# Kernel tuning notes

Hardware: AMD Instinct MI355X
Metric: run time of the kernel (lower is better)

The kernel has to match this reference:

```python
import jax, jax.numpy as jnp
import numpy as np

B, C, HEADS, DH = 2, 1280, 20, 64
INNER = HEADS * DH
HW = 64
S = HW * HW
L = 77
ENC = 4096
GROUPS = 32
EPS = 1e-5
CREG = 1.0     # creg_ in __init__
NOATTN = 1.0   # global noattn
NORES = 1.0    # global noresidual


def setup_inputs() -> dict:
    key = jax.random.key(0)
    ks = jax.random.split(key, 10)
    std = 0.02
    return {
        "x": jax.random.normal(ks[0], (B, C, HW, HW), jnp.float32),
        "text": jax.random.normal(ks[1], (B, L, ENC), jnp.float32),
        "gn_gamma": jnp.ones((C,), jnp.float32),
        "gn_beta": jnp.zeros((C,), jnp.float32),
        "ln_gamma": jnp.ones((ENC,), jnp.float32),
        "ln_beta": jnp.zeros((ENC,), jnp.float32),
        "Wq": jax.random.normal(ks[2], (C, INNER), jnp.float32) * std,
        "bq": jnp.zeros((INNER,), jnp.float32),
        "Wk": jax.random.normal(ks[3], (ENC, INNER), jnp.float32) * std,
        "bk": jnp.zeros((INNER,), jnp.float32),
        "Wv": jax.random.normal(ks[4], (ENC, INNER), jnp.float32) * std,
        "bv": jnp.zeros((INNER,), jnp.float32),
        "Wo": jax.random.normal(ks[5], (INNER, C), jnp.float32) * std,
        "bo": jnp.zeros((C,), jnp.float32),
        "size_reg": jax.random.uniform(ks[6], (1, S, L), jnp.float32),
        "treg": jax.random.uniform(ks[7], (1,), jnp.float32),
        "mask": jax.random.randint(ks[8], (1, S, L), 0, 2, jnp.int32),
    }


def _group_norm(h, gamma, beta):
    # h: [B, C, S]; GroupNorm over (C//GROUPS, S) per group
    hg = h.reshape(B, GROUPS, -1)
    mu = hg.mean(-1, keepdims=True)
    var = hg.var(-1, keepdims=True)
    hn = ((hg - mu) * jax.lax.rsqrt(var + EPS)).reshape(B, C, S)
    return hn * gamma[None, :, None] + beta[None, :, None]


def _layer_norm(t, gamma, beta):
    mu = t.mean(-1, keepdims=True)
    var = t.var(-1, keepdims=True)
    return (t - mu) * jax.lax.rsqrt(var + EPS) * gamma + beta


def reference(x, text, gn_gamma, gn_beta, ln_gamma, ln_beta, Wq, bq, Wk, bk,
              Wv, bv, Wo, bo, size_reg, treg, mask):
    residual = x                              # [B, C, HW, HW]
    h = x.reshape(B, C, S)                    # spatial tokens
    h = _group_norm(h, gn_gamma, gn_beta).transpose(0, 2, 1)   # [B, S, C]
    enc = _layer_norm(text, ln_gamma, ln_beta)                  # [B, L, ENC]

    # head_to_batch_dim (out_dim=3): [B, T, inner] -> [B*heads, T, dh]
    q = (h @ Wq + bq).reshape(B, S, HEADS, DH).transpose(0, 2, 1, 3).reshape(B * HEADS, S, DH)
    k = (enc @ Wk + bk).reshape(B, L, HEADS, DH).transpose(0, 2, 1, 3).reshape(B * HEADS, L, DH)
    v = (enc @ Wv + bv).reshape(B, L, HEADS, DH).transpose(0, 2, 1, 3).reshape(B * HEADS, L, DH)

    scale = DH ** -0.5
    sim = jnp.einsum('bsd,bld->bsl', q, k) * scale            # [B*H, S, L]

    # region regularization applied only to the conditional (second) half
    half = (B * HEADS) // 2
    sim_u, sim_c = sim[:half], sim[half:]
    mn = sim_c.min(-1, keepdims=True)
    mx = sim_c.max(-1, keepdims=True)
    m = mask > 0                                               # [1, S, L] broadcasts over heads
    w = size_reg * CREG * treg[0]
    sim_c = sim_c + jnp.where(m, w, 0.0) * (mx - sim_c) - jnp.where(m, 0.0, w) * (sim_c - mn)
    sim = jnp.concatenate([sim_u, sim_c], axis=0)

    probs = jax.nn.softmax(sim, axis=-1)
    out = jnp.einsum('bsl,bld->bsd', probs, v)                 # [B*H, S, DH]
    # batch_to_head_dim: [B*H, S, DH] -> [B, S, inner]
    out = out.reshape(B, HEADS, S, DH).transpose(0, 2, 1, 3).reshape(B, S, INNER)
    out = out @ Wo + bo                                        # to_out[0]; dropout p=0
    out = out.transpose(0, 2, 1).reshape(residual.shape)       # [B, C, HW, HW]
    return out * NOATTN + residual * NORES
```

## Files before the change

kernel.cpp:

```cpp
#include <hip/hip_runtime.h>

typedef __bf16 bf16_t;
typedef __bf16 bf16x8 __attribute__((ext_vector_type(8)));
typedef float  f32x4  __attribute__((ext_vector_type(4)));
typedef unsigned int u32x4 __attribute__((ext_vector_type(4)));


__global__ __launch_bounds__(256) void k_transpose_cvt2(
    const float* __restrict__ in0, const float* __restrict__ in1,
    bf16_t* __restrict__ out0, bf16_t* __restrict__ out1, int R, int C)
{
  const float* in  = blockIdx.z ? in1 : in0;
  bf16_t*      out = blockIdx.z ? out1 : out0;
  __shared__ float tile[64][33];
  const int c0 = blockIdx.x * 32, r0 = blockIdx.y * 64;
  const int t = threadIdx.x;
#pragma unroll
  for (int it = 0; it < 8; ++it) {
    int r = it * 8 + (t >> 5), c = t & 31;
    tile[r][c] = in[(size_t)(r0 + r) * C + c0 + c];
  }
  __syncthreads();
  {
    const int oc  = t >> 3;
    const int seg = t & 7;
    bf16x8 o;
#pragma unroll
    for (int e = 0; e < 8; ++e) o[e] = (bf16_t)tile[seg * 8 + e][oc];
    *(bf16x8*)(out + (size_t)(c0 + oc) * R + r0 + seg * 8) = o;
  }
}

__global__ __launch_bounds__(256) void k_gn_partial(
    const float* __restrict__ x, float* __restrict__ partial)
{
  const int bg    = blockIdx.x >> 5;
  const int chunk = blockIdx.x & 31;
  const float* p  = x + (size_t)bg * 163840 + (size_t)chunk * 5120;
  float s1 = 0.f, s2 = 0.f;
#pragma unroll
  for (int it = 0; it < 5; ++it) {
    float4 v = *(const float4*)(p + (size_t)(it * 256 + threadIdx.x) * 4);
    s1 += v.x + v.y + v.z + v.w;
    s2 += v.x * v.x + v.y * v.y + v.z * v.z + v.w * v.w;
  }
#pragma unroll
  for (int off = 32; off > 0; off >>= 1) {
    s1 += __shfl_down(s1, off);
    s2 += __shfl_down(s2, off);
  }
  __shared__ float r1[4], r2[4];
  if ((threadIdx.x & 63) == 0) { r1[threadIdx.x >> 6] = s1; r2[threadIdx.x >> 6] = s2; }
  __syncthreads();
  if (threadIdx.x == 0) {
    partial[blockIdx.x * 2]     = r1[0] + r1[1] + r1[2] + r1[3];
    partial[blockIdx.x * 2 + 1] = r2[0] + r2[1] + r2[2] + r2[3];
  }
}

__global__ __launch_bounds__(64) void k_gn_finalize(
    const float* __restrict__ partial, float* __restrict__ stats)
{
  const int bg = threadIdx.x;
  float t1 = 0.f, t2 = 0.f;
#pragma unroll
  for (int c = 0; c < 32; ++c) {
    t1 += partial[(bg * 32 + c) * 2];
    t2 += partial[(bg * 32 + c) * 2 + 1];
  }
  const float invN = 1.0f / 163840.0f;
  float mu  = t1 * invN;
  float var = t2 * invN - mu * mu;
  stats[bg * 2]     = mu;
  stats[bg * 2 + 1] = rsqrtf(var + 1e-5f);
}

__global__ __launch_bounds__(256) void k_gn_apply(
    const float* __restrict__ x, const float* __restrict__ stats,
    const float* __restrict__ gamma, const float* __restrict__ beta,
    bf16_t* __restrict__ h)
{
  __shared__ float tile[64][65];
  const int s0 = blockIdx.x * 64;
  const int c0 = blockIdx.y * 64;
  const int b  = blockIdx.z;
  const int t  = threadIdx.x;
#pragma unroll
  for (int it = 0; it < 16; ++it) {
    int cl = it * 4 + (t >> 6);
    int sl = t & 63;
    tile[cl][sl] = x[((size_t)(b * 1280 + c0 + cl) << 12) + s0 + sl];
  }
  __syncthreads();
#pragma unroll
  for (int it = 0; it < 2; ++it) {
    int i  = it * 256 + t;
    int sl = i >> 3;
    int cg = i & 7;
    bf16x8 o;
#pragma unroll
    for (int e = 0; e < 8; ++e) {
      int c  = c0 + cg * 8 + e;
      int g  = c / 40;
      float mu = stats[(b * 32 + g) * 2];
      float rs = stats[(b * 32 + g) * 2 + 1];
      o[e] = (bf16_t)((tile[cg * 8 + e][sl] - mu) * rs * gamma[c] + beta[c]);
    }
    *(bf16x8*)(h + (size_t)(b * 4096 + s0 + sl) * 1280 + c0 + cg * 8) = o;
  }
}

__global__ __launch_bounds__(256) void k_ln(
    const float* __restrict__ text, const float* __restrict__ g,
    const float* __restrict__ bta, bf16_t* __restrict__ enc)
{
  const int row = blockIdx.x;
  const float* p = text + (size_t)row * 4096;
  float s1 = 0.f, s2 = 0.f;
  for (int i = threadIdx.x; i < 1024; i += 256) {
    float4 v = *(const float4*)(p + (size_t)i * 4);
    s1 += v.x + v.y + v.z + v.w;
    s2 += v.x * v.x + v.y * v.y + v.z * v.z + v.w * v.w;
  }
#pragma unroll
  for (int off = 32; off > 0; off >>= 1) {
    s1 += __shfl_down(s1, off);
    s2 += __shfl_down(s2, off);
  }
  __shared__ float r1[4], r2[4], sh[2];
  if ((threadIdx.x & 63) == 0) { r1[threadIdx.x >> 6] = s1; r2[threadIdx.x >> 6] = s2; }
  __syncthreads();
  if (threadIdx.x == 0) {
    float t1 = r1[0] + r1[1] + r1[2] + r1[3];
    float t2 = r2[0] + r2[1] + r2[2] + r2[3];
    const float invN = 1.0f / 4096.0f;
    float mu  = t1 * invN;
    float var = t2 * invN - mu * mu;
    sh[0] = mu;
    sh[1] = rsqrtf(var + 1e-5f);
  }
  __syncthreads();
  const float mu = sh[0], rs = sh[1];
  for (int i = threadIdx.x; i < 1024; i += 256) {
    float4 v  = *(const float4*)(p + (size_t)i * 4);
    float4 gg = *(const float4*)(g + (size_t)i * 4);
    float4 bb = *(const float4*)(bta + (size_t)i * 4);
    bf16_t* o = enc + (size_t)row * 4096 + (size_t)i * 4;
    o[0] = (bf16_t)((v.x - mu) * rs * gg.x + bb.x);
    o[1] = (bf16_t)((v.y - mu) * rs * gg.y + bb.y);
    o[2] = (bf16_t)((v.z - mu) * rs * gg.z + bb.z);
    o[3] = (bf16_t)((v.w - mu) * rs * gg.w + bb.w);
  }
}

template <int EPI>
__global__ __launch_bounds__(256) void k_gemm(
    const bf16_t* __restrict__ A, const bf16_t* __restrict__ BT,
    const float* __restrict__ bias, bf16_t* __restrict__ outb,
    float* __restrict__ outf, const float* __restrict__ xres,
    float* __restrict__ dout, int M, int lda, int klen)
{
  __shared__ alignas(16) bf16_t smem[4][128 * 64];
  const int tid  = threadIdx.x;
  const int lane = tid & 63;
  const int wv   = tid >> 6;
  const int wm   = wv >> 1, wn = wv & 1;
  const int m0   = blockIdx.x * 128;
  const int n0   = blockIdx.y * 128;
  const int kbeg = blockIdx.z * klen;

  f32x4 acc[4][4];
  const f32x4 fz = {0.f, 0.f, 0.f, 0.f};
#pragma unroll
  for (int i = 0; i < 4; ++i)
#pragma unroll
    for (int j = 0; j < 4; ++j) acc[i][j] = fz;

  auto stage = [&](int buf, int kt) {
#pragma unroll
    for (int it = 0; it < 4; ++it) {
      int slot = it * 256 + tid;
      int row  = slot >> 3, ch = slot & 7;
      int grow = m0 + row; if (grow > M - 1) grow = M - 1;
      const bf16_t* ga = A  + (size_t)grow * lda + kt + ((ch ^ (row & 7)) << 3);
      const bf16_t* gb = BT + (size_t)(n0 + row) * lda + kt + ((ch ^ (row & 7)) << 3);
      __builtin_amdgcn_global_load_lds(
          (const __attribute__((address_space(1))) void*)ga,
          (__attribute__((address_space(3))) void*)((char*)&smem[buf * 2][0] + slot * 16),
          16, 0, 0);
      __builtin_amdgcn_global_load_lds(
          (const __attribute__((address_space(1))) void*)gb,
          (__attribute__((address_space(3))) void*)((char*)&smem[buf * 2 + 1][0] + slot * 16),
          16, 0, 0);
    }
  };

  const int nt = klen >> 6;
  stage(0, kbeg);
  if (nt > 1) stage(1, kbeg + 64);

  for (int t = 0; t < nt; ++t) {
    if (t + 1 < nt) { asm volatile("s_waitcnt vmcnt(8)" ::: "memory"); }
    else            { asm volatile("s_waitcnt vmcnt(0)" ::: "memory"); }
    __builtin_amdgcn_s_barrier();
    const char* pA = (const char*)&smem[(t & 1) * 2][0];
    const char* pB = (const char*)&smem[(t & 1) * 2 + 1][0];
#pragma unroll
    for (int ks = 0; ks < 2; ++ks) {
      const int kb = ks * 64 + ((lane >> 4) << 4);
      bf16x8 af[4], bfg[4];
#pragma unroll
      for (int i = 0; i < 4; ++i) {
        int r = wm * 64 + i * 16 + (lane & 15);
        af[i]  = *(const bf16x8*)(pA + r * 128 + (kb ^ ((r & 7) << 4)));
        int c = wn * 64 + i * 16 + (lane & 15);
        bfg[i] = *(const bf16x8*)(pB + c * 128 + (kb ^ ((c & 7) << 4)));
      }
#pragma unroll
      for (int i = 0; i < 4; ++i)
#pragma unroll
        for (int j = 0; j < 4; ++j)
          acc[i][j] = __builtin_amdgcn_mfma_f32_16x16x32_bf16(af[i], bfg[j], acc[i][j], 0, 0, 0);
    }
    asm volatile("s_waitcnt lgkmcnt(0)" ::: "memory");
    __builtin_amdgcn_s_barrier();
    if (t + 2 < nt) stage(t & 1, kbeg + (t + 2) * 64);
  }

  if (EPI == 0) {
    bf16_t* cst = &smem[0][0];
#pragma unroll
    for (int j = 0; j < 4; ++j) {
      const int n  = n0 + wn * 64 + j * 16 + (lane & 15);
      const float bs = bias[n];
      const int cl = wn * 64 + j * 16 + (lane & 15);
#pragma unroll
      for (int i = 0; i < 4; ++i) {
        const int rl = wm * 64 + i * 16 + ((lane >> 4) << 2);
#pragma unroll
        for (int r = 0; r < 4; ++r)
          cst[(rl + r) * 144 + cl] = (bf16_t)(acc[i][j][r] + bs);
      }
    }
    __syncthreads();
#pragma unroll
    for (int it = 0; it < 8; ++it) {
      int slot = it * 256 + tid;
      int row = slot >> 4, ch = slot & 15;
      u32x4 d = *(const u32x4*)(cst + row * 144 + ch * 8);
      *(u32x4*)(outb + (size_t)(m0 + row) * 1280 + n0 + ch * 8) = d;
    }
  } else {
#pragma unroll
    for (int i = 0; i < 4; ++i) {
      const int mrow = m0 + wm * 64 + i * 16 + ((lane >> 4) << 2);
#pragma unroll
      for (int j = 0; j < 4; ++j) {
        const int n = n0 + wn * 64 + j * 16 + (lane & 15);
        if (EPI == 2) {
          const int b = mrow >> 12, s = mrow & 4095;
          const size_t off = ((size_t)(b * 1280 + n) << 12) + s;
          const float bs = bias[n];
          const float4 xr = *(const float4*)(xres + off);
          float4 o;
          o.x = acc[i][j][0] + bs + xr.x;
          o.y = acc[i][j][1] + bs + xr.y;
          o.z = acc[i][j][2] + bs + xr.z;
          o.w = acc[i][j][3] + bs + xr.w;
          *(float4*)(dout + off) = o;
        } else {
#pragma unroll
          for (int r = 0; r < 4; ++r)
            if (mrow + r < M)
              outf[(size_t)blockIdx.z * (154 * 1280) + (size_t)(mrow + r) * 1280 + n] = acc[i][j][r];
        }
      }
    }
  }
}

__global__ __launch_bounds__(256) void k_kv_reduce(
    const float* __restrict__ part, const float* __restrict__ bias,
    bf16_t* __restrict__ outb)
{
  const int idx = blockIdx.x * 256 + threadIdx.x;
  if (idx >= 154 * 1280) return;
  const int n = idx % 1280;
  float s = bias[n];
#pragma unroll
  for (int sp = 0; sp < 8; ++sp) s += part[(size_t)sp * (154 * 1280) + idx];
  outb[idx] = (bf16_t)s;
}

__global__ __launch_bounds__(256) void k_attn(
    const bf16_t* __restrict__ q, const bf16_t* __restrict__ kbuf,
    const bf16_t* __restrict__ vbuf, bf16_t* __restrict__ ao,
    const float* __restrict__ size_reg, const int* __restrict__ mask,
    const float* __restrict__ treg)
{
  __shared__ alignas(16) bf16_t sQ[64 * 64];
  __shared__ alignas(16) bf16_t sK[80 * 64];
  __shared__ alignas(16) bf16_t sVT[64 * 104];
  __shared__ alignas(16) bf16_t sP[4 * 16 * 104];
  const int s0   = blockIdx.x * 64;
  const int bh   = blockIdx.y;
  const int b    = bh / 20, head = bh % 20;
  const int tid  = threadIdx.x, lane = tid & 63, wv = tid >> 6;
  const int ntok = lane & 15;

  const u32x4 uz = {0u, 0u, 0u, 0u};
  for (int i = tid; i < 832; i += 256) ((u32x4*)sVT)[i] = uz;
  for (int i = tid; i < 832; i += 256) ((u32x4*)sP)[i]  = uz;

  const size_t qbase = ((size_t)(b * 4096 + s0)) * 1280 + head * 64;
  for (int slot = tid; slot < 512; slot += 256) {
    int row = slot >> 3, ch = slot & 7;
    u32x4 d = *(const u32x4*)(q + qbase + (size_t)row * 1280 + ((ch ^ (row & 7)) << 3));
    *(u32x4*)((char*)sQ + slot * 16) = d;
  }
  const size_t kvbase = ((size_t)(b * 77)) * 1280 + head * 64;
  for (int slot = tid; slot < 640; slot += 256) {
    int tok = slot >> 3, ch = slot & 7;
    u32x4 d = uz;
    if (tok < 77)
      d = *(const u32x4*)(kbuf + kvbase + (size_t)tok * 1280 + ((ch ^ (tok & 7)) << 3));
    *(u32x4*)((char*)sK + slot * 16) = d;
  }
  __syncthreads();
  for (int e = tid; e < 77 * 64; e += 256) {
    int tok = e >> 6, dh = e & 63;
    sVT[dh * 104 + tok] = vbuf[kvbase + (size_t)tok * 1280 + dh];
  }
  __syncthreads();

  f32x4 sim[5];
  const f32x4 fz = {0.f, 0.f, 0.f, 0.f};
#pragma unroll
  for (int nf = 0; nf < 5; ++nf) sim[nf] = fz;
  const int qrow = wv * 16 + (lane & 15);
#pragma unroll
  for (int ks = 0; ks < 2; ++ks) {
    const int kb = ks * 64 + ((lane >> 4) << 4);
    bf16x8 aq = *(const bf16x8*)((const char*)sQ + qrow * 128 + (kb ^ ((qrow & 7) << 4)));
#pragma unroll
    for (int nf = 0; nf < 5; ++nf) {
      int tok = nf * 16 + ntok;
      bf16x8 bk = *(const bf16x8*)((const char*)sK + tok * 128 + (kb ^ ((tok & 7) << 4)));
      sim[nf] = __builtin_amdgcn_mfma_f32_16x16x32_bf16(aq, bk, sim[nf], 0, 0, 0);
    }
  }

  float vv[5][4];
#pragma unroll
  for (int nf = 0; nf < 5; ++nf)
#pragma unroll
    for (int r = 0; r < 4; ++r) vv[nf][r] = sim[nf][r] * 0.125f;

  const int rbase = s0 + wv * 16 + ((lane >> 4) << 2);

  if (b == 1) {
    const float tr = treg[0];
#pragma unroll
    for (int r = 0; r < 4; ++r) {
      float mx = -1e30f, mn = 1e30f;
#pragma unroll
      for (int nf = 0; nf < 5; ++nf)
        if (nf * 16 + ntok < 77) { mx = fmaxf(mx, vv[nf][r]); mn = fminf(mn, vv[nf][r]); }
#pragma unroll
      for (int m = 1; m < 16; m <<= 1) {
        mx = fmaxf(mx, __shfl_xor(mx, m));
        mn = fminf(mn, __shfl_xor(mn, m));
      }
      const int srow = rbase + r;
#pragma unroll
      for (int nf = 0; nf < 5; ++nf) {
        int l = nf * 16 + ntok;
        if (l < 77) {
          float w  = size_reg[srow * 77 + l] * tr;
          int   mk = mask[srow * 77 + l];
          float v  = vv[nf][r];
          vv[nf][r] = (mk > 0) ? v + w * (mx - v) : v - w * (v - mn);
        }
      }
    }
  }

#pragma unroll
  for (int r = 0; r < 4; ++r) {
    float mx = -1e30f;
#pragma unroll
    for (int nf = 0; nf < 5; ++nf)
      if (nf * 16 + ntok < 77) mx = fmaxf(mx, vv[nf][r]);
#pragma unroll
    for (int m = 1; m < 16; m <<= 1) mx = fmaxf(mx, __shfl_xor(mx, m));
    float p[5]; float sm = 0.f;
#pragma unroll
    for (int nf = 0; nf < 5; ++nf) {
      bool val = (nf * 16 + ntok) < 77;
      p[nf] = val ? __expf(vv[nf][r] - mx) : 0.f;
      sm += p[nf];
    }
#pragma unroll
    for (int m = 1; m < 16; m <<= 1) sm += __shfl_xor(sm, m);
    const float inv = 1.0f / sm;
    const int prow = ((lane >> 4) << 2) + r;
#pragma unroll
    for (int nf = 0; nf < 5; ++nf)
      sP[wv * 1664 + prow * 104 + nf * 16 + ntok] = (bf16_t)(p[nf] * inv);
  }
  __syncthreads();

  f32x4 o[4];
#pragma unroll
  for (int fd = 0; fd < 4; ++fd) o[fd] = fz;
#pragma unroll
  for (int ks = 0; ks < 3; ++ks) {
    const int kb = ks * 64 + ((lane >> 4) << 4);
    bf16x8 ap = *(const bf16x8*)((const char*)sP + wv * 3328 + (lane & 15) * 208 + kb);
#pragma unroll
    for (int fd = 0; fd < 4; ++fd) {
      bf16x8 bv = *(const bf16x8*)((const char*)sVT + (fd * 16 + (lane & 15)) * 208 + kb);
      o[fd] = __builtin_amdgcn_mfma_f32_16x16x32_bf16(ap, bv, o[fd], 0, 0, 0);
    }
  }
  const size_t obase =
      ((size_t)(b * 4096 + s0 + wv * 16 + ((lane >> 4) << 2))) * 1280 + head * 64;
#pragma unroll
  for (int fd = 0; fd < 4; ++fd)
#pragma unroll
    for (int r = 0; r < 4; ++r)
      ao[obase + (size_t)r * 1280 + fd * 16 + (lane & 15)] = (bf16_t)o[fd][r];
}

extern "C" void kernel_launch(void* const* d_in, const int* in_sizes, int n_in,
                              void* d_out, int out_size, void* d_ws, size_t ws_size,
                              hipStream_t stream)
{
  const float* x    = (const float*)d_in[0];
  const float* text = (const float*)d_in[1];
  const float* gng  = (const float*)d_in[2];
  const float* gnb  = (const float*)d_in[3];
  const float* lng  = (const float*)d_in[4];
  const float* lnb  = (const float*)d_in[5];
  const float* Wq   = (const float*)d_in[6];
  const float* bq   = (const float*)d_in[7];
  const float* Wk   = (const float*)d_in[8];
  const float* bk   = (const float*)d_in[9];
  const float* Wv   = (const float*)d_in[10];
  const float* bv   = (const float*)d_in[11];
  const float* Wo   = (const float*)d_in[12];
  const float* bo   = (const float*)d_in[13];
  const float* sreg = (const float*)d_in[14];
  const float* treg = (const float*)d_in[15];
  const int*   msk  = (const int*)d_in[16];
  float* out = (float*)d_out;

  char* ws = (char*)d_ws;
  size_t off = 0;
  auto alloc = [&](size_t bytes) {
    char* p = ws + off;
    off += (bytes + 255) & ~(size_t)255;
    return p;
  };
  float*  partial = (float*)alloc(2048 * 2 * sizeof(float));
  float*  stats   = (float*)alloc(64 * 2 * sizeof(float));
  bf16_t* WqT = (bf16_t*)alloc((size_t)1280 * 1280 * 2);
  bf16_t* WkT = (bf16_t*)alloc((size_t)1280 * 4096 * 2);
  bf16_t* WvT = (bf16_t*)alloc((size_t)1280 * 4096 * 2);
  bf16_t* WoT = (bf16_t*)alloc((size_t)1280 * 1280 * 2);
  bf16_t* h   = (bf16_t*)alloc((size_t)8192 * 1280 * 2);
  bf16_t* enc = (bf16_t*)alloc((size_t)154 * 4096 * 2);
  bf16_t* qb  = (bf16_t*)alloc((size_t)8192 * 1280 * 2);
  bf16_t* kb  = (bf16_t*)alloc((size_t)154 * 1280 * 2);
  bf16_t* vb  = (bf16_t*)alloc((size_t)154 * 1280 * 2);
  float*  part = (float*)alloc((size_t)8 * 154 * 1280 * sizeof(float));

  k_transpose_cvt2<<<dim3(40, 20, 2),  256, 0, stream>>>(Wq, Wo, WqT, WoT, 1280, 1280);
  k_transpose_cvt2<<<dim3(40, 64, 2), 256, 0, stream>>>(Wk, Wv, WkT, WvT, 4096, 1280);

  k_gn_partial<<<2048, 256, 0, stream>>>(x, partial);
  k_gn_finalize<<<1, 64, 0, stream>>>(partial, stats);
  k_gn_apply<<<dim3(64, 20, 2), 256, 0, stream>>>(x, stats, gng, gnb, h);
  k_ln<<<154, 256, 0, stream>>>(text, lng, lnb, enc);

  k_gemm<0><<<dim3(64, 10), 256, 0, stream>>>(h, WqT, bq, qb, nullptr, nullptr, nullptr, 8192, 1280, 1280);
  k_gemm<1><<<dim3(2, 10, 8), 256, 0, stream>>>(enc, WkT, nullptr, nullptr, part, nullptr, nullptr, 154, 4096, 512);
  k_kv_reduce<<<770, 256, 0, stream>>>(part, bk, kb);
  k_gemm<1><<<dim3(2, 10, 8), 256, 0, stream>>>(enc, WvT, nullptr, nullptr, part, nullptr, nullptr, 154, 4096, 512);
  k_kv_reduce<<<770, 256, 0, stream>>>(part, bv, vb);

  k_attn<<<dim3(64, 40), 256, 0, stream>>>(qb, kb, vb, h, sreg, msk, treg);

  k_gemm<2><<<dim3(64, 10), 256, 0, stream>>>(h, WoT, bo, nullptr, nullptr, x, out, 8192, 1280, 1280);
}
```

Measured before the change: 184.6 us.

## Use 128x64 GEMM tiles with XCD-aware block remap and fused K/V projection

The GEMM tile shrinks from 128x128 to 128x64, with a smaller LDS footprint and a launch-bounds hint to fit more blocks per CU. Blocks are launched on a 1D grid and remapped so consecutive tiles land on the same XCD, which should improve L2 reuse. The K and V projections now run as one split-K launch over 2560 output columns, followed by a single merged reduce. That merge relies on WkT and WvT sitting next to each other in the workspace. Smaller tiles lower per-block operand reuse in exchange for better occupancy and wave balance.

```diff
diff --git a/kernel.cpp b/kernel.cpp
--- a/kernel.cpp
+++ b/kernel.cpp
@@ -154,100 +154,114 @@
 }
 
 template <int EPI>
-__global__ __launch_bounds__(256) void k_gemm(
+__global__ __launch_bounds__(256, 3) void k_gemm(
     const bf16_t* __restrict__ A, const bf16_t* __restrict__ BT,
     const float* __restrict__ bias, bf16_t* __restrict__ outb,
     float* __restrict__ outf, const float* __restrict__ xres,
-    float* __restrict__ dout, int M, int lda, int klen)
-{
-  __shared__ alignas(16) bf16_t smem[4][128 * 64];
+    float* __restrict__ dout, int M, int lda, int klen, int nnt, int nst)
+{
+  __shared__ alignas(16) bf16_t smem[24576];
   const int tid  = threadIdx.x;
   const int lane = tid & 63;
   const int wv   = tid >> 6;
   const int wm   = wv >> 1, wn = wv & 1;
-  const int m0   = blockIdx.x * 128;
-  const int n0   = blockIdx.y * 128;
+
+  const int cpx  = gridDim.x >> 3;
+  const int nbid = (blockIdx.x & 7) * cpx + (blockIdx.x >> 3);
+  const int mt   = nbid / nnt, ntile = nbid % nnt;
+  const int m0   = mt * 128;
+  const int n0   = ntile * 64;
   const int kbeg = blockIdx.z * klen;
 
-  f32x4 acc[4][4];
+  f32x4 acc[4][2];
   const f32x4 fz = {0.f, 0.f, 0.f, 0.f};
 #pragma unroll
   for (int i = 0; i < 4; ++i)
 #pragma unroll
-    for (int j = 0; j < 4; ++j) acc[i][j] = fz;
+    for (int j = 0; j < 2; ++j) acc[i][j] = fz;
 
   auto stage = [&](int buf, int kt) {
+    bf16_t* sA = smem + buf * 8192;
+    bf16_t* sB = smem + 16384 + buf * 4096;
 #pragma unroll
     for (int it = 0; it < 4; ++it) {
       int slot = it * 256 + tid;
       int row  = slot >> 3, ch = slot & 7;
       int grow = m0 + row; if (grow > M - 1) grow = M - 1;
-      const bf16_t* ga = A  + (size_t)grow * lda + kt + ((ch ^ (row & 7)) << 3);
+      const bf16_t* ga = A + (size_t)grow * lda + kt + ((ch ^ (row & 7)) << 3);
+      __builtin_amdgcn_global_load_lds(
+          (const __attribute__((address_space(1))) void*)ga,
+          (__attribute__((address_space(3))) void*)((char*)sA + slot * 16),
+          16, 0, 0);
+    }
+#pragma unroll
+    for (int it = 0; it < 2; ++it) {
+      int slot = it * 256 + tid;
+      int row  = slot >> 3, ch = slot & 7;
       const bf16_t* gb = BT + (size_t)(n0 + row) * lda + kt + ((ch ^ (row & 7)) << 3);
       __builtin_amdgcn_global_load_lds(
-          (const __attribute__((address_space(1))) void*)ga,
-          (__attribute__((address_space(3))) void*)((char*)&smem[buf * 2][0] + slot * 16),
+          (const __attribute__((address_space(1))) void*)gb,
+          (__attribute__((address_space(3))) void*)((char*)sB + slot * 16),
           16, 0, 0);
-      __builtin_amdgcn_global_load_lds(
-          (const __attribute__((address_space(1))) void*)gb,
-          (__attribute__((address_space(3))) void*)((char*)&smem[buf * 2 + 1][0] + slot * 16),
-          16, 0, 0);
     }
   };
 
-  const int nt = klen >> 6;
+  const int nt_k = klen >> 6;
   stage(0, kbeg);
-  if (nt > 1) stage(1, kbeg + 64);
-
-  for (int t = 0; t < nt; ++t) {
-    if (t + 1 < nt) { asm volatile("s_waitcnt vmcnt(8)" ::: "memory"); }
-    else            { asm volatile("s_waitcnt vmcnt(0)" ::: "memory"); }
+  if (nt_k > 1) stage(1, kbeg + 64);
+
+  for (int t = 0; t < nt_k; ++t) {
+    if (t + 1 < nt_k) { asm volatile("s_waitcnt vmcnt(6)" ::: "memory"); }
+    else              { asm volatile("s_waitcnt vmcnt(0)" ::: "memory"); }
     __builtin_amdgcn_s_barrier();
-    const char* pA = (const char*)&smem[(t & 1) * 2][0];
-    const char* pB = (const char*)&smem[(t & 1) * 2 + 1][0];
+    const char* pA = (const char*)(smem + (t & 1) * 8192);
+    const char* pB = (const char*)(smem + 16384 + (t & 1) * 4096);
 #pragma unroll
     for (int ks = 0; ks < 2; ++ks) {
       const int kb = ks * 64 + ((lane >> 4) << 4);
-      bf16x8 af[4], bfg[4];
+      bf16x8 af[4], bfg[2];
 #pragma unroll
       for (int i = 0; i < 4; ++i) {
         int r = wm * 64 + i * 16 + (lane & 15);
-        af[i]  = *(const bf16x8*)(pA + r * 128 + (kb ^ ((r & 7) << 4)));
-        int c = wn * 64 + i * 16 + (lane & 15);
-        bfg[i] = *(const bf16x8*)(pB + c * 128 + (kb ^ ((c & 7) << 4)));
+        af[i] = *(const bf16x8*)(pA + r * 128 + (kb ^ ((r & 7) << 4)));
       }
 #pragma unroll
+      for (int j = 0; j < 2; ++j) {
+        int c = wn * 32 + j * 16 + (lane & 15);
+        bfg[j] = *(const bf16x8*)(pB + c * 128 + (kb ^ ((c & 7) << 4)));
+      }
+#pragma unroll
       for (int i = 0; i < 4; ++i)
 #pragma unroll
-        for (int j = 0; j < 4; ++j)
+        for (int j = 0; j < 2; ++j)
           acc[i][j] = __builtin_amdgcn_mfma_f32_16x16x32_bf16(af[i], bfg[j], acc[i][j], 0, 0, 0);
     }
     asm volatile("s_waitcnt lgkmcnt(0)" ::: "memory");
     __builtin_amdgcn_s_barrier();
-    if (t + 2 < nt) stage(t & 1, kbeg + (t + 2) * 64);
+    if (t + 2 < nt_k) stage(t & 1, kbeg + (t + 2) * 64);
   }
 
   if (EPI == 0) {
-    bf16_t* cst = &smem[0][0];
-#pragma unroll
-    for (int j = 0; j < 4; ++j) {
-      const int n  = n0 + wn * 64 + j * 16 + (lane & 15);
+    bf16_t* cst = smem;
+#pragma unroll
+    for (int j = 0; j < 2; ++j) {
+      const int n  = n0 + wn * 32 + j * 16 + (lane & 15);
       const float bs = bias[n];
-      const int cl = wn * 64 + j * 16 + (lane & 15);
+      const int cl = wn * 32 + j * 16 + (lane & 15);
 #pragma unroll
       for (int i = 0; i < 4; ++i) {
         const int rl = wm * 64 + i * 16 + ((lane >> 4) << 2);
 #pragma unroll
         for (int r = 0; r < 4; ++r)
-          cst[(rl + r) * 144 + cl] = (bf16_t)(acc[i][j][r] + bs);
+          cst[(rl + r) * 76 + cl] = (bf16_t)(acc[i][j][r] + bs);
       }
     }
     __syncthreads();
 #pragma unroll
-    for (int it = 0; it < 8; ++it) {
+    for (int it = 0; it < 4; ++it) {
       int slot = it * 256 + tid;
-      int row = slot >> 4, ch = slot & 15;
-      u32x4 d = *(const u32x4*)(cst + row * 144 + ch * 8);
+      int row = slot >> 3, ch = slot & 7;
+      u32x4 d = *(const u32x4*)(cst + row * 76 + ch * 8);
       *(u32x4*)(outb + (size_t)(m0 + row) * 1280 + n0 + ch * 8) = d;
     }
   } else {
@@ -255,8 +269,8 @@
     for (int i = 0; i < 4; ++i) {
       const int mrow = m0 + wm * 64 + i * 16 + ((lane >> 4) << 2);
 #pragma unroll
-      for (int j = 0; j < 4; ++j) {
-        const int n = n0 + wn * 64 + j * 16 + (lane & 15);
+      for (int j = 0; j < 2; ++j) {
+        const int n = n0 + wn * 32 + j * 16 + (lane & 15);
         if (EPI == 2) {
           const int b = mrow >> 12, s = mrow & 4095;
           const size_t off = ((size_t)(b * 1280 + n) << 12) + s;
@@ -272,7 +286,7 @@
 #pragma unroll
           for (int r = 0; r < 4; ++r)
             if (mrow + r < M)
-              outf[(size_t)blockIdx.z * (154 * 1280) + (size_t)(mrow + r) * 1280 + n] = acc[i][j][r];
+              outf[(size_t)blockIdx.z * 154 * nst + (size_t)(mrow + r) * nst + n] = acc[i][j][r];
         }
       }
     }
@@ -280,16 +294,17 @@
 }
 
 __global__ __launch_bounds__(256) void k_kv_reduce(
-    const float* __restrict__ part, const float* __restrict__ bias,
-    bf16_t* __restrict__ outb)
+    const float* __restrict__ part, const float* __restrict__ bk,
+    const float* __restrict__ bv, bf16_t* __restrict__ kb, bf16_t* __restrict__ vb)
 {
   const int idx = blockIdx.x * 256 + threadIdx.x;
-  if (idx >= 154 * 1280) return;
-  const int n = idx % 1280;
-  float s = bias[n];
-#pragma unroll
-  for (int sp = 0; sp < 8; ++sp) s += part[(size_t)sp * (154 * 1280) + idx];
-  outb[idx] = (bf16_t)s;
+  if (idx >= 154 * 2560) return;
+  const int r = idx / 2560, n = idx % 2560;
+  float s = (n < 1280) ? bk[n] : bv[n - 1280];
+#pragma unroll
+  for (int sp = 0; sp < 8; ++sp) s += part[(size_t)sp * (154 * 2560) + idx];
+  if (n < 1280) kb[(size_t)r * 1280 + n] = (bf16_t)s;
+  else          vb[(size_t)r * 1280 + n - 1280] = (bf16_t)s;
 }
 
 __global__ __launch_bounds__(256) void k_attn(
@@ -473,9 +488,9 @@
   bf16_t* qb  = (bf16_t*)alloc((size_t)8192 * 1280 * 2);
   bf16_t* kb  = (bf16_t*)alloc((size_t)154 * 1280 * 2);
   bf16_t* vb  = (bf16_t*)alloc((size_t)154 * 1280 * 2);
-  float*  part = (float*)alloc((size_t)8 * 154 * 1280 * sizeof(float));
-
-  k_transpose_cvt2<<<dim3(40, 20, 2),  256, 0, stream>>>(Wq, Wo, WqT, WoT, 1280, 1280);
+  float*  part = (float*)alloc((size_t)8 * 154 * 2560 * sizeof(float));
+
+  k_transpose_cvt2<<<dim3(40, 20, 2), 256, 0, stream>>>(Wq, Wo, WqT, WoT, 1280, 1280);
   k_transpose_cvt2<<<dim3(40, 64, 2), 256, 0, stream>>>(Wk, Wv, WkT, WvT, 4096, 1280);
 
   k_gn_partial<<<2048, 256, 0, stream>>>(x, partial);
@@ -483,13 +498,14 @@
   k_gn_apply<<<dim3(64, 20, 2), 256, 0, stream>>>(x, stats, gng, gnb, h);
   k_ln<<<154, 256, 0, stream>>>(text, lng, lnb, enc);
 
-  k_gemm<0><<<dim3(64, 10), 256, 0, stream>>>(h, WqT, bq, qb, nullptr, nullptr, nullptr, 8192, 1280, 1280);
-  k_gemm<1><<<dim3(2, 10, 8), 256, 0, stream>>>(enc, WkT, nullptr, nullptr, part, nullptr, nullptr, 154, 4096, 512);
-  k_kv_reduce<<<770, 256, 0, stream>>>(part, bk, kb);
-  k_gemm<1><<<dim3(2, 10, 8), 256, 0, stream>>>(enc, WvT, nullptr, nullptr, part, nullptr, nullptr, 154, 4096, 512);
-  k_kv_reduce<<<770, 256, 0, stream>>>(part, bv, vb);
+  k_gemm<0><<<dim3(1280), 256, 0, stream>>>(h, WqT, bq, qb, nullptr, nullptr, nullptr,
+                                            8192, 1280, 1280, 20, 1280);
+  k_gemm<1><<<dim3(80, 1, 8), 256, 0, stream>>>(enc, WkT, nullptr, nullptr, part, nullptr, nullptr,
+                                                154, 4096, 512, 40, 2560);
+  k_kv_reduce<<<1540, 256, 0, stream>>>(part, bk, bv, kb, vb);
 
   k_attn<<<dim3(64, 40), 256, 0, stream>>>(qb, kb, vb, h, sreg, msk, treg);
 
-  k_gemm<2><<<dim3(64, 10), 256, 0, stream>>>(h, WoT, bo, nullptr, nullptr, x, out, 8192, 1280, 1280);
-}
+  k_gemm<2><<<dim3(1280), 256, 0, stream>>>(h, WoT, bo, nullptr, nullptr, x, out,
+                                            8192, 1280, 1280, 20, 1280);
+}
```

Result: faster. 175.1 us (-5.1%).
